# Performance work log

Hardware: AMD Instinct MI355X
Metric: run time of the kernel (lower is better)

Reference implementation:

```python
import jax, jax.numpy as jnp
from jax import lax
import numpy as np

# Module hyperparameters (match init_kwargs)
N = 4            # number of multiplex cells per feature map
NUM_FM = 64      # feature maps in the input
NF = N * NUM_FM  # lateral channel count = 256
H = W = 32       # feature map height/width
D = 2            # lateral neighborhood radius
PRD = 2          # padding repair distance (must equal D for symmetric pad)
KS = 2 * D + 1   # lateral kernel size = 5
IOTA = 0.1       # blend of activation vs lateral support for winner selection
B = 16           # batch size


def minmax_fm(x):
    """Min-max normalize each feature map (over the last two dims) to [0,1].
    Degenerate (constant) maps map to 0."""
    mn = jnp.min(x, axis=(-2, -1), keepdims=True)
    mx = jnp.max(x, axis=(-2, -1), keepdims=True)
    denom = mx - mn
    safe = jnp.where(denom > 0, denom, 1.0)
    return jnp.where(denom > 0, (x - mn) / safe, 0.0)


def _pad(A):
    # pad_activations: zeros of shape (.., PRD+D+H, PRD+D+W), A at [PRD:-PRD]
    # with PRD == D this is symmetric (PRD, D) padding.
    return jnp.pad(A, ((0, 0), (0, 0), (PRD, D), (PRD, D)))


def _conv(x, w):
    # x: (B, Cin, H', W'), w: (Cout, Cin, KS, KS) -> VALID conv (padding=0)
    return lax.conv_general_dilated(x, w, (1, 1), 'VALID',
                                    dimension_numbers=('NCHW', 'OIHW', 'NCHW'))


def setup_inputs() -> dict:
    key = jax.random.key(0)
    k1, k2 = jax.random.split(key)
    A = jax.random.uniform(k1, (B, NUM_FM, H, W), dtype=jnp.float32)
    K = jax.random.normal(k2, (NF, NF, KS, KS), dtype=jnp.float32)  # trained lateral kernel
    S = jnp.ones((NF,), dtype=jnp.float32)                          # scaling param
    return {"A": A, "K": K, "S": S}


def reference(A, K, S):
    batch = A.shape[0]
    # A.repeat(1, n, 1, 1): tile input n times along channels -> (B, NF, H, W)
    A_rep = jnp.tile(A, (1, N, 1, 1))

    # First lateral pass: conv with minmax-normalized K^T, scaled by S, minmaxed.
    L1 = _conv(_pad(A_rep), minmax_fm(jnp.swapaxes(K, 0, 1))) / NUM_FM
    L1 = L1 * S[None, :, None, None]
    L1 = minmax_fm(L1)

    # Winner-take-all multiplex selection (deterministic branch):
    s = jnp.sum((1.0 - IOTA) * A_rep + IOTA * L1, axis=(-2, -1))  # (B, NF)
    s = jnp.swapaxes(s.reshape(batch, N, NUM_FM), 1, 2)            # (B, NUM_FM, N)
    A_max = jnp.argmax(s, axis=-1)                                  # (B, NUM_FM)
    fm_idx = NUM_FM * A_max + jnp.arange(NUM_FM)                    # (B, NUM_FM) channel ids

    # Active-channel mask (complement = inactive_multiplex_idx in the original)
    active = jnp.zeros((batch, NF), dtype=bool)
    active = active.at[jnp.arange(batch)[:, None], fm_idx].set(True)

    # Zero inactive channels of A (tmp_A) and diagonal K[i,i] for inactive i
    # (large_K[b, idx, idx] = 0 is pairwise/diagonal fancy indexing in torch).
    tmp_A = A_rep * active[:, :, None, None].astype(A_rep.dtype)
    eye = jnp.eye(NF, dtype=bool)
    kill = eye[None, :, :] & (~active)[:, :, None]                  # (B, NF, NF)
    large_K = jnp.where(kill[..., None, None], 0.0, K[None])        # (B, NF, NF, KS, KS)

    # Second lateral pass: per-sample conv with per-sample kernel.
    pA = _pad(tmp_A)

    def per_sample(x, Kb):
        w = minmax_fm(jnp.swapaxes(Kb, 0, 1))
        return _conv(x[None], w)[0]

    L2 = jax.vmap(per_sample)(pA, large_K) / NUM_FM                 # (B, NF, H, W)

    # Gather winning channels: filtered_L (B, NUM_FM, H, W)
    return jnp.take_along_axis(L2, fm_idx[:, :, None, None], axis=1)
```

## Files before the change

kernel.cpp:

```cpp
#include <hip/hip_runtime.h>


#define NFM 64
#define NMX 4
#define NFC 256
#define HW 1024
#define KK 25

typedef unsigned short u16;
typedef short short8 __attribute__((ext_vector_type(8)));
typedef float f32x4 __attribute__((ext_vector_type(4)));

__device__ __forceinline__ u16 f2bfbits(float f) {
    unsigned int u = __float_as_uint(f);
    u += 0x7fffu + ((u >> 16) & 1u);
    return (u16)(u >> 16);
}
__device__ __forceinline__ float bf2f(u16 v) {
    return __uint_as_float(((unsigned int)v) << 16);
}

__global__ __launch_bounds__(256) void kprep(const float* __restrict__ K,
                                             float* __restrict__ wsum2) {
    __shared__ __align__(16) float buf[64 * KK];
    int g = blockIdx.x & 63, o0 = (blockIdx.x >> 6) * 64;
    int t = threadIdx.x;
    float wacc[KK];
#pragma unroll
    for (int k = 0; k < KK; ++k) wacc[k] = 0.f;

    for (int n = 0; n < NMX; ++n) {
        int i = n * NFM + g;
        const float4* src = (const float4*)(K + (i * NFC + o0) * KK);
        __syncthreads();
        ((float4*)buf)[t] = src[t];
        if (t < 144) ((float4*)buf)[t + 256] = src[t + 256];
        __syncthreads();
        if (t < 64) {
            float v[KK];
            float mn = 1e30f, mx = -1e30f;
#pragma unroll
            for (int k = 0; k < KK; ++k) {
                v[k] = buf[t * KK + k];
                mn = fminf(mn, v[k]);
                mx = fmaxf(mx, v[k]);
            }
            float d = mx - mn;
            float r = d > 0.f ? 1.f / d : 0.f;
#pragma unroll
            for (int k = 0; k < KK; ++k) wacc[k] += (v[k] - mn) * r;
        }
    }
    __syncthreads();
    if (t < 64) {
#pragma unroll
        for (int k = 0; k < KK; ++k) buf[t * KK + k] = wacc[k];
    }
    __syncthreads();
    for (int idx = t; idx < 1600; idx += 256) {
        int k = idx >> 6, ol = idx & 63;
        wsum2[(g * KK + k) * NFC + o0 + ol] = buf[ol * KK + k];
    }
}

__global__ __launch_bounds__(256) void kpackW(const float* __restrict__ wsum2,
                                              char* __restrict__ Wpk) {
    __shared__ float wlds[64 * 16];
    int dydx = blockIdx.x, ot = blockIdx.y, t = threadIdx.x;
    int o15 = t & 15, gq = t >> 4;
#pragma unroll
    for (int e = 0; e < 4; ++e) {
        int g = e * 16 + gq;
        wlds[g * 16 + o15] = wsum2[(g * KK + dydx) * NFC + ot * 16 + o15];
    }
    __syncthreads();
    int gh = t >> 7, l = t & 63;
    int quad = l >> 4, oo = l & 15;
    short8 hs, ls;
#pragma unroll
    for (int j = 0; j < 8; ++j) {
        float v = wlds[(gh * 32 + quad * 8 + j) * 16 + oo];
        u16 h = f2bfbits(v);
        hs[j] = (short)h;
        ls[j] = (short)f2bfbits(v - bf2f(h));
    }
    char* cb = Wpk + (ot * 50 + dydx * 2 + gh) * 2048 + l * 16;
    *(short8*)cb = hs;
    *(short8*)(cb + 1024) = ls;
}

__global__ __launch_bounds__(512, 4) void kscore(const float* __restrict__ A,
                                                 const char* __restrict__ Wpk,
                                                 float* __restrict__ part) {
    __shared__ u16 slabh[5 * 36 * 72];
    __shared__ u16 slabl[5 * 36 * 72];
    int t = threadIdx.x;
    int y = blockIdx.x, b = blockIdx.y;
    int lane = t & 63;
    int wv = __builtin_amdgcn_readfirstlane(t >> 6);
    int n15 = lane & 15, quad = lane >> 4;

    const float* Ab = A + b * NFM * HW;
    for (int ry = 0; ry < 5; ++ry) {
        int gy = y - 2 + ry;
        bool rowok = (gy >= 0) && (gy < 32);
        for (int c = 0; c < 5; ++c) {
            int id2 = c * 512 + t;
            if (id2 < 2304) {
                int g = (id2 * 3641) >> 17;
                int xi = id2 - g * 36;
                float v = 0.f;
                if (rowok && xi >= 2 && xi < 34)
                    v = Ab[g * HW + gy * 32 + xi - 2];
                u16 h = f2bfbits(v);
                u16 l = f2bfbits(v - bf2f(h));
                int idx = (ry * 36 + xi) * 72 + g;
                slabh[idx] = h;
                slabl[idx] = l;
            }
        }
    }
    __syncthreads();

    f32x4 acc[2][2];
#pragma unroll
    for (int m = 0; m < 2; ++m)
#pragma unroll
        for (int p = 0; p < 2; ++p)
#pragma unroll
            for (int r = 0; r < 4; ++r) acc[m][p][r] = 0.f;

    const char* wbase0 = Wpk + (wv * 2) * 50 * 2048 + lane * 16;
    const char* wbase1 = wbase0 + 50 * 2048;
    short8 cah0 = *(const short8*)(wbase0);
    short8 cal0 = *(const short8*)(wbase0 + 1024);
    short8 cah1 = *(const short8*)(wbase1);
    short8 cal1 = *(const short8*)(wbase1 + 1024);

    for (int ks = 0; ks < 50; ++ks) {
        int ksn = ks < 49 ? ks + 1 : 49;
        const char* nb0 = wbase0 + (ksn << 11);
        const char* nb1 = wbase1 + (ksn << 11);
        short8 nah0 = *(const short8*)nb0;
        short8 nal0 = *(const short8*)(nb0 + 1024);
        short8 nah1 = *(const short8*)nb1;
        short8 nal1 = *(const short8*)(nb1 + 1024);

        int dydx = ks >> 1;
        int gh = (ks & 1) * 32;
        int dy = dydx / 5, dx = dydx - dy * 5;
        short8 bh[2], bl[2];
#pragma unroll
        for (int p = 0; p < 2; ++p) {
            int addr = (dy * 36 + p * 16 + n15 + dx) * 72 + gh + quad * 8;
            bh[p] = *(const short8*)(slabh + addr);
            bl[p] = *(const short8*)(slabl + addr);
        }
#pragma unroll
        for (int p = 0; p < 2; ++p) {
            acc[0][p] = __builtin_amdgcn_mfma_f32_16x16x32_bf16(cah0, bh[p], acc[0][p], 0, 0, 0);
            acc[0][p] = __builtin_amdgcn_mfma_f32_16x16x32_bf16(cah0, bl[p], acc[0][p], 0, 0, 0);
            acc[0][p] = __builtin_amdgcn_mfma_f32_16x16x32_bf16(cal0, bh[p], acc[0][p], 0, 0, 0);
            acc[1][p] = __builtin_amdgcn_mfma_f32_16x16x32_bf16(cah1, bh[p], acc[1][p], 0, 0, 0);
            acc[1][p] = __builtin_amdgcn_mfma_f32_16x16x32_bf16(cah1, bl[p], acc[1][p], 0, 0, 0);
            acc[1][p] = __builtin_amdgcn_mfma_f32_16x16x32_bf16(cal1, bh[p], acc[1][p], 0, 0, 0);
        }
        cah0 = nah0; cal0 = nal0; cah1 = nah1; cal1 = nal1;
    }

#pragma unroll
    for (int m = 0; m < 2; ++m) {
#pragma unroll
        for (int reg = 0; reg < 4; ++reg) {
            float v0 = acc[m][0][reg], v1 = acc[m][1][reg];
            float mn = fminf(v0, v1);
            float mx = fmaxf(v0, v1);
            float sm = v0 + v1;
#pragma unroll
            for (int msk = 1; msk <= 8; msk <<= 1) {
                mn = fminf(mn, __shfl_xor(mn, msk, 64));
                mx = fmaxf(mx, __shfl_xor(mx, msk, 64));
                sm += __shfl_xor(sm, msk, 64);
            }
            if (n15 == 0) {
                int o = (wv * 2 + m) * 16 + quad * 4 + reg;
                float* pd = part + ((b * NFC + o) * 32 + y) * 3;
                pd[0] = mn; pd[1] = mx; pd[2] = sm;
            }
        }
    }
}

__global__ __launch_bounds__(256) void kfin(const float* __restrict__ part,
                                            const float* __restrict__ S,
                                            int* __restrict__ ig) {
    __shared__ float scl[NFC];
    int b = blockIdx.x, t = threadIdx.x;
    const float* pp = part + (b * NFC + t) * 96;
    float mn = 1e30f, mx = -1e30f, sm = 0.f;
#pragma unroll
    for (int r = 0; r < 32; ++r) {
        mn = fminf(mn, pp[r * 3]);
        mx = fmaxf(mx, pp[r * 3 + 1]);
        sm += pp[r * 3 + 2];
    }
    float s = S[t] * (1.f / 64.f);
    float mnv = (s >= 0.f ? mn : mx) * s;
    float mxv = (s >= 0.f ? mx : mn) * s;
    float smv = sm * s;
    float d = mxv - mnv;
    scl[t] = d > 0.f ? (smv - 1024.f * mnv) / d : 0.f;
    __syncthreads();
    if (t < NFM) {
        float best = scl[t];
        int bi = 0;
#pragma unroll
        for (int n = 1; n < NMX; ++n) {
            float v = scl[n * NFM + t];
            if (v > best) { best = v; bi = n; }
        }
        ig[b * NFM + t] = bi * NFM + t;
    }
}

__global__ __launch_bounds__(256) void kpackO(const float* __restrict__ K,
                                              const int* __restrict__ ig,
                                              char* __restrict__ Wob) {
    __shared__ int igL[NFM];
    __shared__ __align__(16) char cbuf[25 * 2048];
    int ft = blockIdx.x, b = blockIdx.y;
    int t = threadIdx.x;
    if (t < NFM) igL[t] = ig[b * NFM + t];
    __syncthreads();
    int g32 = t & 31, fh = t >> 5;
    int quad = g32 >> 3, j = g32 & 7;
    char* wdst = Wob + b * 409600 + ft * 102400;

    for (int half = 0; half < 2; ++half) {
        int i = igL[half * 32 + g32];
#pragma unroll
        for (int e = 0; e < 2; ++e) {
            int f15 = fh * 2 + e;
            int o = igL[ft * 16 + f15];
            const float* src = K + (i * NFC + o) * KK;
            float v[KK];
            float mn = 1e30f, mx = -1e30f;
#pragma unroll
            for (int k = 0; k < KK; ++k) {
                v[k] = src[k];
                mn = fminf(mn, v[k]);
                mx = fmaxf(mx, v[k]);
            }
            float d = mx - mn;
            float r = d > 0.f ? 1.f / d : 0.f;
            char* base = cbuf + (quad * 16 + f15) * 16 + j * 2;
#pragma unroll
            for (int k = 0; k < KK; ++k) {
                float nv = (v[k] - mn) * r;
                u16 h = f2bfbits(nv);
                u16 l = f2bfbits(nv - bf2f(h));
                *(u16*)(base + k * 2048) = h;
                *(u16*)(base + k * 2048 + 1024) = l;
            }
        }
        __syncthreads();
        for (int idx = t; idx < 3200; idx += 256) {
            int ch = idx >> 7, w = idx & 127;
            *(float4*)(wdst + (ch * 2 + half) * 2048 + w * 16) =
                *(const float4*)(cbuf + ch * 2048 + w * 16);
        }
        __syncthreads();
    }
}

__global__ __launch_bounds__(256, 4) void kout(const float* __restrict__ A,
                                               const char* __restrict__ Wob,
                                               float* __restrict__ out) {
    __shared__ u16 slabh[6 * 20 * 72];
    __shared__ u16 slabl[6 * 20 * 72];
    int t = threadIdx.x;
    int xh = blockIdx.x, yb2 = blockIdx.y, b = blockIdx.z;
    int y0 = yb2 * 2, x0 = xh * 16;
    int lane = t & 63;
    int wv = __builtin_amdgcn_readfirstlane(t >> 6);
    int n15 = lane & 15, quad = lane >> 4;

    const float* Ab = A + b * NFM * HW;
    for (int ry = 0; ry < 6; ++ry) {
        int gy = y0 - 2 + ry;
        bool rowok = (gy >= 0) && (gy < 32);
        for (int c = 0; c < 5; ++c) {
            int id2 = c * 256 + t;
            int g = (id2 * 6554) >> 17;
            int xi = id2 - g * 20;
            int x = x0 + xi - 2;
            float v = 0.f;
            if (rowok && x >= 0 && x < 32)
                v = Ab[g * HW + gy * 32 + x];
            u16 h = f2bfbits(v);
            u16 l = f2bfbits(v - bf2f(h));
            int idx = (ry * 20 + xi) * 72 + g;
            slabh[idx] = h;
            slabl[idx] = l;
        }
    }
    __syncthreads();

    f32x4 acc[2];
#pragma unroll
    for (int r = 0; r < 2; ++r)
#pragma unroll
        for (int jr = 0; jr < 4; ++jr) acc[r][jr] = 0.f;

    const char* wbase = Wob + b * 409600 + (wv * 50) * 2048 + lane * 16;
    short8 cah = *(const short8*)(wbase);
    short8 cal = *(const short8*)(wbase + 1024);

    for (int ks = 0; ks < 50; ++ks) {
        int ksn = ks < 49 ? ks + 1 : 49;
        const char* nb = wbase + (ksn << 11);
        short8 nah = *(const short8*)nb;
        short8 nal = *(const short8*)(nb + 1024);

        int dydx = ks >> 1;
        int gh = (ks & 1) * 32;
        int dy = dydx / 5, dx = dydx - dy * 5;
#pragma unroll
        for (int r = 0; r < 2; ++r) {
            int addr = ((r + dy) * 20 + n15 + dx) * 72 + gh + quad * 8;
            short8 bh = *(const short8*)(slabh + addr);
            short8 bl = *(const short8*)(slabl + addr);
            acc[r] = __builtin_amdgcn_mfma_f32_16x16x32_bf16(cah, bh, acc[r], 0, 0, 0);
            acc[r] = __builtin_amdgcn_mfma_f32_16x16x32_bf16(cah, bl, acc[r], 0, 0, 0);
            acc[r] = __builtin_amdgcn_mfma_f32_16x16x32_bf16(cal, bh, acc[r], 0, 0, 0);
        }
        cah = nah;
        cal = nal;
    }

#pragma unroll
    for (int r = 0; r < 2; ++r)
#pragma unroll
        for (int reg = 0; reg < 4; ++reg) {
            int f = wv * 16 + quad * 4 + reg;
            out[(b * NFM + f) * HW + (y0 + r) * 32 + x0 + n15] = acc[r][reg] * (1.f / 64.f);
        }
}

extern "C" void kernel_launch(void* const* d_in, const int* in_sizes, int n_in,
                              void* d_out, int out_size, void* d_ws, size_t ws_size,
                              hipStream_t stream) {
    const float* A = (const float*)d_in[0];
    const float* K = (const float*)d_in[1];
    const float* S = (const float*)d_in[2];
    float* out = (float*)d_out;

    char* ws = (char*)d_ws;
    char*   Wob   = ws;
    char*   Wpk   = ws;
    float*  wsum2 = (float*)(ws + 1638400);
    float*  part  = (float*)(ws + 6553600);
    int*    igv   = (int*)(ws + 8126464);

    kprep<<<dim3(256), dim3(256), 0, stream>>>(K, wsum2);
    kpackW<<<dim3(25, 16), dim3(256), 0, stream>>>(wsum2, Wpk);
    kscore<<<dim3(32, 16), dim3(512), 0, stream>>>(A, Wpk, part);
    kfin<<<dim3(16), dim3(256), 0, stream>>>(part, S, igv);
    kpackO<<<dim3(4, 16), dim3(256), 0, stream>>>(K, igv, Wob);
    kout<<<dim3(2, 16, 16), dim3(256), 0, stream>>>(A, Wob, out);
}
```

Measured before the change: 161.2 us.

## Compute two output rows per score block and fuse winner selection into packing

The score kernel now computes two output rows per block, so each A-weight fragment loaded from global memory feeds twice as many MFMAs. This halves the weight traffic and the block count, at the cost of a larger LDS slab and more accumulators (launch bounds drop to 2 blocks per CU). The separate finalize kernel is removed and its winner selection is recomputed inside each kpackO block from float4 partials. That saves a launch but repeats the reduction in all 4 blocks per batch.

```diff
diff --git a/kernel.cpp b/kernel.cpp
--- a/kernel.cpp
+++ b/kernel.cpp
@@ -89,20 +89,21 @@
     *(short8*)(cb + 1024) = ls;
 }
 
-__global__ __launch_bounds__(512, 4) void kscore(const float* __restrict__ A,
+__global__ __launch_bounds__(512, 2) void kscore(const float* __restrict__ A,
                                                  const char* __restrict__ Wpk,
-                                                 float* __restrict__ part) {
-    __shared__ u16 slabh[5 * 36 * 72];
-    __shared__ u16 slabl[5 * 36 * 72];
+                                                 float4* __restrict__ part) {
+    __shared__ u16 slabh[6 * 36 * 72];
+    __shared__ u16 slabl[6 * 36 * 72];
     int t = threadIdx.x;
-    int y = blockIdx.x, b = blockIdx.y;
+    int y2 = blockIdx.x, b = blockIdx.y;
+    int y0 = y2 * 2;
     int lane = t & 63;
     int wv = __builtin_amdgcn_readfirstlane(t >> 6);
     int n15 = lane & 15, quad = lane >> 4;
 
     const float* Ab = A + b * NFM * HW;
-    for (int ry = 0; ry < 5; ++ry) {
-        int gy = y - 2 + ry;
+    for (int ry = 0; ry < 6; ++ry) {
+        int gy = y0 - 2 + ry;
         bool rowok = (gy >= 0) && (gy < 32);
         for (int c = 0; c < 5; ++c) {
             int id2 = c * 512 + t;
@@ -122,11 +123,11 @@
     }
     __syncthreads();
 
-    f32x4 acc[2][2];
+    f32x4 acc[2][4];
 #pragma unroll
     for (int m = 0; m < 2; ++m)
 #pragma unroll
-        for (int p = 0; p < 2; ++p)
+        for (int p = 0; p < 4; ++p)
 #pragma unroll
             for (int r = 0; r < 4; ++r) acc[m][p][r] = 0.f;
 
@@ -149,15 +150,16 @@
         int dydx = ks >> 1;
         int gh = (ks & 1) * 32;
         int dy = dydx / 5, dx = dydx - dy * 5;
-        short8 bh[2], bl[2];
-#pragma unroll
-        for (int p = 0; p < 2; ++p) {
-            int addr = (dy * 36 + p * 16 + n15 + dx) * 72 + gh + quad * 8;
+        short8 bh[4], bl[4];
+#pragma unroll
+        for (int p = 0; p < 4; ++p) {
+            int r = p >> 1, nt = p & 1;
+            int addr = ((r + dy) * 36 + nt * 16 + n15 + dx) * 72 + gh + quad * 8;
             bh[p] = *(const short8*)(slabh + addr);
             bl[p] = *(const short8*)(slabl + addr);
         }
 #pragma unroll
-        for (int p = 0; p < 2; ++p) {
+        for (int p = 0; p < 4; ++p) {
             acc[0][p] = __builtin_amdgcn_mfma_f32_16x16x32_bf16(cah0, bh[p], acc[0][p], 0, 0, 0);
             acc[0][p] = __builtin_amdgcn_mfma_f32_16x16x32_bf16(cah0, bl[p], acc[0][p], 0, 0, 0);
             acc[0][p] = __builtin_amdgcn_mfma_f32_16x16x32_bf16(cal0, bh[p], acc[0][p], 0, 0, 0);
@@ -173,9 +175,10 @@
 #pragma unroll
         for (int reg = 0; reg < 4; ++reg) {
             float v0 = acc[m][0][reg], v1 = acc[m][1][reg];
-            float mn = fminf(v0, v1);
-            float mx = fmaxf(v0, v1);
-            float sm = v0 + v1;
+            float v2 = acc[m][2][reg], v3 = acc[m][3][reg];
+            float mn = fminf(fminf(v0, v1), fminf(v2, v3));
+            float mx = fmaxf(fmaxf(v0, v1), fmaxf(v2, v3));
+            float sm = (v0 + v1) + (v2 + v3);
 #pragma unroll
             for (int msk = 1; msk <= 8; msk <<= 1) {
                 mn = fminf(mn, __shfl_xor(mn, msk, 64));
@@ -184,54 +187,51 @@
             }
             if (n15 == 0) {
                 int o = (wv * 2 + m) * 16 + quad * 4 + reg;
-                float* pd = part + ((b * NFC + o) * 32 + y) * 3;
-                pd[0] = mn; pd[1] = mx; pd[2] = sm;
-            }
-        }
-    }
-}
-
-__global__ __launch_bounds__(256) void kfin(const float* __restrict__ part,
-                                            const float* __restrict__ S,
-                                            int* __restrict__ ig) {
+                part[(b * NFC + o) * 16 + y2] = make_float4(mn, mx, sm, 0.f);
+            }
+        }
+    }
+}
+
+__global__ __launch_bounds__(256) void kpackO(const float* __restrict__ K,
+                                              const float4* __restrict__ part,
+                                              const float* __restrict__ S,
+                                              char* __restrict__ Wob) {
     __shared__ float scl[NFC];
-    int b = blockIdx.x, t = threadIdx.x;
-    const float* pp = part + (b * NFC + t) * 96;
-    float mn = 1e30f, mx = -1e30f, sm = 0.f;
-#pragma unroll
-    for (int r = 0; r < 32; ++r) {
-        mn = fminf(mn, pp[r * 3]);
-        mx = fmaxf(mx, pp[r * 3 + 1]);
-        sm += pp[r * 3 + 2];
-    }
-    float s = S[t] * (1.f / 64.f);
-    float mnv = (s >= 0.f ? mn : mx) * s;
-    float mxv = (s >= 0.f ? mx : mn) * s;
-    float smv = sm * s;
-    float d = mxv - mnv;
-    scl[t] = d > 0.f ? (smv - 1024.f * mnv) / d : 0.f;
-    __syncthreads();
-    if (t < NFM) {
-        float best = scl[t];
-        int bi = 0;
-#pragma unroll
-        for (int n = 1; n < NMX; ++n) {
-            float v = scl[n * NFM + t];
-            if (v > best) { best = v; bi = n; }
-        }
-        ig[b * NFM + t] = bi * NFM + t;
-    }
-}
-
-__global__ __launch_bounds__(256) void kpackO(const float* __restrict__ K,
-                                              const int* __restrict__ ig,
-                                              char* __restrict__ Wob) {
     __shared__ int igL[NFM];
     __shared__ __align__(16) char cbuf[25 * 2048];
     int ft = blockIdx.x, b = blockIdx.y;
     int t = threadIdx.x;
-    if (t < NFM) igL[t] = ig[b * NFM + t];
-    __syncthreads();
+    {
+        const float4* pp = part + (b * NFC + t) * 16;
+        float mn = 1e30f, mx = -1e30f, sm = 0.f;
+#pragma unroll
+        for (int r = 0; r < 16; ++r) {
+            float4 p = pp[r];
+            mn = fminf(mn, p.x);
+            mx = fmaxf(mx, p.y);
+            sm += p.z;
+        }
+        float s = S[t] * (1.f / 64.f);
+        float mnv = (s >= 0.f ? mn : mx) * s;
+        float mxv = (s >= 0.f ? mx : mn) * s;
+        float smv = sm * s;
+        float d = mxv - mnv;
+        scl[t] = d > 0.f ? (smv - 1024.f * mnv) / d : 0.f;
+    }
+    __syncthreads();
+    if (t < NFM) {
+        float best = scl[t];
+        int bi = 0;
+#pragma unroll
+        for (int n = 1; n < NMX; ++n) {
+            float v = scl[n * NFM + t];
+            if (v > best) { best = v; bi = n; }
+        }
+        igL[t] = bi * NFM + t;
+    }
+    __syncthreads();
+
     int g32 = t & 31, fh = t >> 5;
     int quad = g32 >> 3, j = g32 & 7;
     char* wdst = Wob + b * 409600 + ft * 102400;
@@ -359,13 +359,11 @@
     char*   Wob   = ws;
     char*   Wpk   = ws;
     float*  wsum2 = (float*)(ws + 1638400);
-    float*  part  = (float*)(ws + 6553600);
-    int*    igv   = (int*)(ws + 8126464);
+    float4* part  = (float4*)(ws + 6553600);
 
     kprep<<<dim3(256), dim3(256), 0, stream>>>(K, wsum2);
     kpackW<<<dim3(25, 16), dim3(256), 0, stream>>>(wsum2, Wpk);
-    kscore<<<dim3(32, 16), dim3(512), 0, stream>>>(A, Wpk, part);
-    kfin<<<dim3(16), dim3(256), 0, stream>>>(part, S, igv);
-    kpackO<<<dim3(4, 16), dim3(256), 0, stream>>>(K, igv, Wob);
+    kscore<<<dim3(16, 16), dim3(512), 0, stream>>>(A, Wpk, part);
+    kpackO<<<dim3(4, 16), dim3(256), 0, stream>>>(K, part, S, Wob);
     kout<<<dim3(2, 16, 16), dim3(256), 0, stream>>>(A, Wob, out);
 }
```

Measured after the change: 150.4 us. 6.7% less time.
